# Optimization experiments

Measured on AMD Instinct MI355X. Metric: run time of the kernel, lower is better.

Reference implementation:

```python
import jax, jax.numpy as jnp
import numpy as np

VOCAB = 30001
EMB = 256
HID = 512          # bidirectional total; 256 per direction
NTAG = 9
B, L = 64, 512


def setup_inputs() -> dict:
    key = jax.random.key(0)
    ks = jax.random.split(key, 12)
    Hd = HID // 2
    s = 0.1
    return {
        "x": jax.random.randint(ks[0], (B, L), 0, VOCAB),
        "embed": jax.random.normal(ks[1], (VOCAB, EMB), jnp.float32) * s,
        "W_ih_f": jax.random.normal(ks[2], (4 * Hd, EMB), jnp.float32) * s,
        "W_hh_f": jax.random.normal(ks[3], (4 * Hd, Hd), jnp.float32) * s,
        "b_f": jax.random.normal(ks[4], (4 * Hd,), jnp.float32) * s,
        "W_ih_b": jax.random.normal(ks[5], (4 * Hd, EMB), jnp.float32) * s,
        "W_hh_b": jax.random.normal(ks[6], (4 * Hd, Hd), jnp.float32) * s,
        "b_b": jax.random.normal(ks[7], (4 * Hd,), jnp.float32) * s,
        "W_out": jax.random.normal(ks[8], (NTAG, HID), jnp.float32) * s,
        "b_out": jax.random.normal(ks[9], (NTAG,), jnp.float32) * s,
        "start_trans": jax.random.normal(ks[10], (NTAG,), jnp.float32) * s,
        "trans": jax.random.normal(ks[11], (NTAG, NTAG), jnp.float32) * s,
        "end_trans": jax.random.normal(jax.random.fold_in(key, 99), (NTAG,), jnp.float32) * s,
    }


def _lstm_dir(xg, W_hh, reverse):
    # xg: [L, B, 4H] precomputed input-to-gate projections (+ bias)
    Hd = W_hh.shape[1]
    nB = xg.shape[1]
    h0 = jnp.zeros((nB, Hd), xg.dtype)
    c0 = jnp.zeros((nB, Hd), xg.dtype)

    def step(carry, gx):
        h, c = carry
        g = gx + h @ W_hh.T                     # [B, 4H]
        i, f, gg, o = jnp.split(g, 4, axis=-1)  # torch gate order i,f,g,o
        c = jax.nn.sigmoid(f) * c + jax.nn.sigmoid(i) * jnp.tanh(gg)
        h = jax.nn.sigmoid(o) * jnp.tanh(c)
        return (h, c), h

    _, hs = jax.lax.scan(step, (h0, c0), xg, reverse=reverse)
    return hs  # [L, B, H]


def _viterbi(emissions, start, trans, end):
    # emissions: [L, B, T]. Max-plus DP (torchcrf CRF.decode, no mask).
    score0 = start + emissions[0]  # [B, T]

    def step(score, em_t):
        # score[b, i] + trans[i, j] + em_t[b, j]
        nxt = score[:, :, None] + trans[None] + em_t[:, None, :]
        return jnp.max(nxt, axis=1), jnp.argmax(nxt, axis=1)

    score, history = jax.lax.scan(step, score0, emissions[1:])  # history: [L-1, B, T]
    score = score + end
    last = jnp.argmax(score, axis=-1)   # [B] best tag at position L-1
    best = jnp.max(score, axis=-1)      # [B] best path score

    def back(tag, idx_t):
        prev = jnp.take_along_axis(idx_t, tag[:, None], axis=1)[:, 0]
        return prev, prev

    _, tags_head = jax.lax.scan(back, last, history, reverse=True)  # [L-1, B]
    tags = jnp.concatenate([tags_head, last[None]], axis=0)         # [L, B]
    return tags.T, best


def reference(x, embed, W_ih_f, W_hh_f, b_f, W_ih_b, W_hh_b, b_b,
              W_out, b_out, start_trans, trans, end_trans):
    xt = x.T                              # [L, B] time-first
    emb = embed[xt]                       # [L, B, E]
    gx_f = jnp.einsum('lbe,ge->lbg', emb, W_ih_f) + b_f
    gx_b = jnp.einsum('lbe,ge->lbg', emb, W_ih_b) + b_b
    hf = _lstm_dir(gx_f, W_hh_f, reverse=False)
    hb = _lstm_dir(gx_b, W_hh_b, reverse=True)
    outputs = jnp.concatenate([hf, hb], axis=-1)            # [L, B, HID]
    emissions = jnp.einsum('lbh,th->lbt', outputs, W_out) + b_out  # [L, B, T]
    tags, best = _viterbi(emissions, start_trans, trans, end_trans)
    return tags, best
```

## Files before the change

kernel.cpp:

```cpp
#include <hip/hip_runtime.h>
#include <math.h>


#define Bv 64
#define Lv 512

__device__ __forceinline__ float sigmoidf_(float x) { return 1.0f / (1.0f + expf(-x)); }

__global__ __launch_bounds__(256, 1) void lstm_persist(
    const int* __restrict__ x, const float* __restrict__ embed,
    const float* __restrict__ Wih_f, const float* __restrict__ Whh_f, const float* __restrict__ bf,
    const float* __restrict__ Wih_b, const float* __restrict__ Whh_b, const float* __restrict__ bb_,
    float* __restrict__ h_glob, int* __restrict__ tags, float* __restrict__ h_hist)
{
    const int bid = blockIdx.x;
    const int d  = bid >> 7;
    const int ug = (bid >> 2) & 31;
    const int bg = bid & 3;
    const int g  = d * 4 + bg;
    const int tid = threadIdx.x;
    const int u0 = ug * 8;
    const int b0 = bg * 16;

    const float* Wih  = d ? Wih_b : Wih_f;
    const float* Whh  = d ? Whh_b : Whh_f;
    const float* bias = d ? bb_   : bf;

    const int ks = tid >> 5;
    const int tr = (tid >> 2) & 7;
    const int tb = tid & 3;
    const int k0 = ks * 32;

    __shared__ float wih_lds[32][260];
    __shared__ float h_lds[16][260];
    __shared__ float emb_lds[2][16][260];
    __shared__ float parts[4][32][17];
    __shared__ float bias_lds[32];

    {
        const int row = tid >> 3;
        const int seg = tid & 7;
        const int gq = row >> 3, j = row & 7;
        const float4* src = reinterpret_cast<const float4*>(
            Wih + ((size_t)(gq * 256 + u0 + j)) * 256 + seg * 32);
        float4* dst = reinterpret_cast<float4*>(&wih_lds[row][seg * 32]);
        #pragma unroll
        for (int q = 0; q < 8; ++q) dst[q] = src[q];
    }
    if (tid < 32) bias_lds[tid] = bias[(tid >> 3) * 256 + u0 + (tid & 7)];

    float4 whh[4][8];
    #pragma unroll
    for (int i = 0; i < 4; ++i) {
        const float* wr = Whh + ((size_t)(i * 256 + u0 + tr)) * 256 + k0;
        #pragma unroll
        for (int m = 0; m < 8; ++m) whh[i][m] = *reinterpret_cast<const float4*>(wr + 4 * m);
    }

    float creg = 0.f;
    const int* my_tag = tags + g * 32 + (tid >> 3);
    int* rel_tag = tags + g * 32 + ug;

    {
        const int b = tid >> 4;
        const int cseg = tid & 15;
        const int t_eff0 = d ? (Lv - 1) : 0;
        const int xv = x[(b0 + b) * Lv + t_eff0];
        const float4* src = reinterpret_cast<const float4*>(embed + (size_t)xv * 256 + cseg * 16);
        float4* dstp = reinterpret_cast<float4*>(&emb_lds[0][b][cseg * 16]);
        dstp[0] = src[0]; dstp[1] = src[1]; dstp[2] = src[2]; dstp[3] = src[3];
    }
    __syncthreads();

    for (int tt = 0; tt < Lv; ++tt) {
        const int par = tt & 1;

        float acc[4][4];
        #pragma unroll
        for (int i = 0; i < 4; ++i)
            #pragma unroll
            for (int u = 0; u < 4; ++u) acc[i][u] = 0.f;

        #pragma unroll
        for (int m = 0; m < 8; ++m) {
            float4 ev[4];
            #pragma unroll
            for (int u = 0; u < 4; ++u)
                ev[u] = *reinterpret_cast<const float4*>(&emb_lds[par][tb + 4 * u][k0 + 4 * m]);
            #pragma unroll
            for (int i = 0; i < 4; ++i) {
                float4 wv = *reinterpret_cast<const float4*>(&wih_lds[tr + 8 * i][k0 + 4 * m]);
                #pragma unroll
                for (int u = 0; u < 4; ++u)
                    acc[i][u] += wv.x * ev[u].x + wv.y * ev[u].y + wv.z * ev[u].z + wv.w * ev[u].w;
            }
        }

        if (tt + 1 < Lv) {
            const int b = tid >> 4;
            const int cseg = tid & 15;
            const int t_eff1 = d ? (Lv - 2 - tt) : (tt + 1);
            const int xv = x[(b0 + b) * Lv + t_eff1];
            const float4* src = reinterpret_cast<const float4*>(embed + (size_t)xv * 256 + cseg * 16);
            float4 e0 = src[0], e1 = src[1], e2 = src[2], e3 = src[3];
            float4* dstp = reinterpret_cast<float4*>(&emb_lds[par ^ 1][b][cseg * 16]);
            dstp[0] = e0; dstp[1] = e1; dstp[2] = e2; dstp[3] = e3;
        }

        if (tt > 0) {
            int v, it = 0;
            for (;;) {
                asm volatile("global_load_dword %0, %1, off sc0 sc1\n\t"
                             "s_waitcnt vmcnt(0)"
                             : "=v"(v) : "v"(my_tag) : "memory");
                if (v >= tt) break;
                if (++it > (1 << 22)) break;
            }
            const float* hs = h_glob + ((size_t)par * 8 + g) * 4096 + tid * 16;
            float4 a0, a1, a2, a3;
            asm volatile(
                "global_load_dwordx4 %0, %4, off sc0 sc1\n\t"
                "global_load_dwordx4 %1, %4, off offset:16 sc0 sc1\n\t"
                "global_load_dwordx4 %2, %4, off offset:32 sc0 sc1\n\t"
                "global_load_dwordx4 %3, %4, off offset:48 sc0 sc1\n\t"
                "s_waitcnt vmcnt(0)"
                : "=v"(a0), "=v"(a1), "=v"(a2), "=v"(a3)
                : "v"(hs) : "memory");
            __builtin_amdgcn_sched_barrier(0);
            const int u = tid;
            h_lds[ 0][u] = a0.x; h_lds[ 1][u] = a0.y; h_lds[ 2][u] = a0.z; h_lds[ 3][u] = a0.w;
            h_lds[ 4][u] = a1.x; h_lds[ 5][u] = a1.y; h_lds[ 6][u] = a1.z; h_lds[ 7][u] = a1.w;
            h_lds[ 8][u] = a2.x; h_lds[ 9][u] = a2.y; h_lds[10][u] = a2.z; h_lds[11][u] = a2.w;
            h_lds[12][u] = a3.x; h_lds[13][u] = a3.y; h_lds[14][u] = a3.z; h_lds[15][u] = a3.w;
        }
        __syncthreads();

        if (tt > 0) {
            #pragma unroll
            for (int m = 0; m < 8; ++m) {
                float4 hv[4];
                #pragma unroll
                for (int u = 0; u < 4; ++u)
                    hv[u] = *reinterpret_cast<const float4*>(&h_lds[tb + 4 * u][k0 + 4 * m]);
                #pragma unroll
                for (int i = 0; i < 4; ++i) {
                    float4 wv = whh[i][m];
                    #pragma unroll
                    for (int u = 0; u < 4; ++u)
                        acc[i][u] += wv.x * hv[u].x + wv.y * hv[u].y + wv.z * hv[u].z + wv.w * hv[u].w;
                }
            }
        }

        #pragma unroll
        for (int i = 0; i < 4; ++i)
            #pragma unroll
            for (int u = 0; u < 4; ++u)
                acc[i][u] += __shfl_xor(acc[i][u], 32);
        if ((tid & 32) == 0) {
            const int w = tid >> 6;
            #pragma unroll
            for (int i = 0; i < 4; ++i)
                #pragma unroll
                for (int u = 0; u < 4; ++u)
                    parts[w][tr + 8 * i][tb + 4 * u] = acc[i][u];
        }
        __syncthreads();

        if (tid < 128) {
            const int j  = tid & 7;
            const int bb = tid >> 3;
            const int t_eff = d ? (Lv - 1 - tt) : tt;
            float gv[4];
            #pragma unroll
            for (int q = 0; q < 4; ++q) {
                const int r = q * 8 + j;
                gv[q] = parts[0][r][bb] + parts[1][r][bb] + parts[2][r][bb] + parts[3][r][bb]
                      + bias_lds[r];
            }
            creg = sigmoidf_(gv[1]) * creg + sigmoidf_(gv[0]) * tanhf(gv[2]);
            const float h = sigmoidf_(gv[3]) * tanhf(creg);
            float* dst = h_glob + ((size_t)(par ^ 1) * 8 + g) * 4096
                       + (size_t)(u0 + j) * 16 + bb;
            asm volatile("global_store_dword %0, %1, off sc0 sc1"
                         :: "v"(dst), "v"(h) : "memory");
            h_hist[((size_t)(b0 + bb) * Lv + t_eff) * 512 + d * 256 + u0 + j] = h;
        }
        asm volatile("s_waitcnt vmcnt(0)" ::: "memory");
        __syncthreads();
        if (tid == 0) {
            int val = tt + 1;
            asm volatile("global_store_dword %0, %1, off sc0 sc1"
                         :: "v"(rel_tag), "v"(val) : "memory");
        }
    }
}

__global__ __launch_bounds__(256) void emis_kernel(
    const float* __restrict__ h_hist, const float* __restrict__ Wout,
    const float* __restrict__ bout, float* __restrict__ em)
{
    const int l  = blockIdx.x >> 2;
    const int bg = blockIdx.x & 3;
    const int tid = threadIdx.x;
    __shared__ float w_lds[9][516];
    __shared__ float h_ldsx[16][512];

    for (int i = tid; i < 9 * 512; i += 256) w_lds[i >> 9][i & 511] = Wout[i];
    for (int i = tid; i < 16 * 128; i += 256) {
        const int bb = i >> 7; const int k = (i & 127) * 4;
        *reinterpret_cast<float4*>(&h_ldsx[bb][k]) =
            *reinterpret_cast<const float4*>(&h_hist[((size_t)(bg * 16 + bb) * 512 + l) * 512 + k]);
    }
    __syncthreads();

    const int bb = tid >> 4;
    const int j = tid & 15;
    if (j < 9) {
        float acc = bout[j];
        #pragma unroll 4
        for (int k = 0; k < 512; k += 4) {
            float4 hv = *reinterpret_cast<const float4*>(&h_ldsx[bb][k]);
            float4 wv = *reinterpret_cast<const float4*>(&w_lds[j][k]);
            acc += hv.x * wv.x + hv.y * wv.y + hv.z * wv.z + hv.w * wv.w;
        }
        em[((size_t)l * 64 + bg * 16 + bb) * 9 + j] = acc;
    }
}

__global__ __launch_bounds__(576) void viterbi_fwd(
    const float* __restrict__ em, const float* __restrict__ start,
    const float* __restrict__ trans, const float* __restrict__ endt,
    unsigned char* __restrict__ hist, int* __restrict__ last_tag,
    float* __restrict__ out_best)
{
    const int tid = threadIdx.x;
    const int b = tid / 9;
    const int j = tid - b * 9;
    __shared__ float sc[2][64][9];
    float t9[9];
    #pragma unroll
    for (int i = 0; i < 9; ++i) t9[i] = trans[i * 9 + j];

    sc[0][b][j] = start[j] + em[tid];
    float emv = em[(64 + b) * 9 + j];
    __syncthreads();
    for (int t = 1; t < 512; ++t) {
        float em_nxt = (t < 511) ? em[((t + 1) * 64 + b) * 9 + j] : 0.f;
        const int cur = t & 1, prv = cur ^ 1;
        float best = -1e30f; int arg = 0;
        #pragma unroll
        for (int i = 0; i < 9; ++i) {
            float v = sc[prv][b][i] + t9[i];
            if (v > best) { best = v; arg = i; }
        }
        best += emv;
        sc[cur][b][j] = best;
        hist[((size_t)b * 512 + t) * 9 + j] = (unsigned char)arg;
        __syncthreads();
        emv = em_nxt;
    }
    sc[1][b][j] += endt[j];
    __syncthreads();
    if (j == 0) {
        float best = -1e30f; int arg = 0;
        #pragma unroll
        for (int i = 0; i < 9; ++i) {
            float v = sc[1][b][i];
            if (v > best) { best = v; arg = i; }
        }
        out_best[b] = best;
        last_tag[b] = arg;
    }
}

__global__ __launch_bounds__(256) void backtrack(
    const unsigned char* __restrict__ hist, const int* __restrict__ last_tag,
    float* __restrict__ out_tags)
{
    const int b = blockIdx.x;
    const int tid = threadIdx.x;
    __shared__ __align__(16) unsigned char hl[512 * 9];
    const uint4* src = reinterpret_cast<const uint4*>(hist + (size_t)b * 512 * 9);
    uint4* dst = reinterpret_cast<uint4*>(hl);
    for (int i = tid; i < 512 * 9 / 16; i += 256) dst[i] = src[i];
    __syncthreads();
    if (tid == 0) {
        int tag = last_tag[b];
        out_tags[b * 512 + 511] = (float)tag;
        for (int t = 511; t >= 1; --t) {
            tag = hl[t * 9 + tag];
            out_tags[b * 512 + t - 1] = (float)tag;
        }
    }
}

extern "C" void kernel_launch(void* const* d_in, const int* in_sizes, int n_in,
                              void* d_out, int out_size, void* d_ws, size_t ws_size,
                              hipStream_t stream)
{
    const int*   x     = (const int*)d_in[0];
    const float* embed = (const float*)d_in[1];
    const float* Wih_f = (const float*)d_in[2];
    const float* Whh_f = (const float*)d_in[3];
    const float* bf    = (const float*)d_in[4];
    const float* Wih_b = (const float*)d_in[5];
    const float* Whh_b = (const float*)d_in[6];
    const float* bb    = (const float*)d_in[7];
    const float* Wout  = (const float*)d_in[8];
    const float* bout  = (const float*)d_in[9];
    const float* start = (const float*)d_in[10];
    const float* trans = (const float*)d_in[11];
    const float* endt  = (const float*)d_in[12];

    char* ws = (char*)d_ws;
    float* h_glob = (float*)ws;
    int*   tags   = (int*)(ws + 262144);
    float* h_hist = (float*)(ws + 266240);
    float* em     = (float*)(ws + 266240 + 67108864);
    int*   last_tag = (int*)(ws + 67375104 + 1179648);
    unsigned char* hist = (unsigned char*)(ws + 68554752 + 256);

    float* out = (float*)d_out;

    hipMemsetAsync(tags, 0, 4096, stream);

    lstm_persist<<<256, 256, 0, stream>>>(x, embed, Wih_f, Whh_f, bf,
                                          Wih_b, Whh_b, bb,
                                          h_glob, tags, h_hist);
    emis_kernel<<<2048, 256, 0, stream>>>(h_hist, Wout, bout, em);
    viterbi_fwd<<<1, 576, 0, stream>>>(em, start, trans, endt, hist, last_tag, out + 64 * 512);
    backtrack<<<64, 256, 0, stream>>>(hist, last_tag, out);
}
```

Before: 2.852 ms.

## Rework persistent LSTM cross-block sync with per-wave flags and double-buffered h

Reassigns block IDs so blocks of the same group are interleaved, and double-buffers the shared h tile so the block-wide barrier before releasing the step flag can be dropped. Each wave now publishes its own progress flag (four per block), and consumers poll all four with a single vector load, sleeping briefly after a few failed polls. The h_hist store is moved after the flag release so it leaves the critical path, and the cell update is spread over even threads in all waves. The aim is lower per-timestep synchronization latency in the 512-step recurrence, at the cost of more complex flag ordering and slightly more LDS.

```diff
diff --git a/kernel.cpp b/kernel.cpp
--- a/kernel.cpp
+++ b/kernel.cpp
@@ -14,10 +14,10 @@
     float* __restrict__ h_glob, int* __restrict__ tags, float* __restrict__ h_hist)
 {
     const int bid = blockIdx.x;
-    const int d  = bid >> 7;
-    const int ug = (bid >> 2) & 31;
-    const int bg = bid & 3;
-    const int g  = d * 4 + bg;
+    const int g  = bid & 7;
+    const int d  = g >> 2;
+    const int bg = g & 3;
+    const int ug = bid >> 3;
     const int tid = threadIdx.x;
     const int u0 = ug * 8;
     const int b0 = bg * 16;
@@ -32,7 +32,7 @@
     const int k0 = ks * 32;
 
     __shared__ float wih_lds[32][260];
-    __shared__ float h_lds[16][260];
+    __shared__ float h_lds[2][16][260];
     __shared__ float emb_lds[2][16][260];
     __shared__ float parts[4][32][17];
     __shared__ float bias_lds[32];
@@ -56,10 +56,6 @@
         #pragma unroll
         for (int m = 0; m < 8; ++m) whh[i][m] = *reinterpret_cast<const float4*>(wr + 4 * m);
     }
-
-    float creg = 0.f;
-    const int* my_tag = tags + g * 32 + (tid >> 3);
-    int* rel_tag = tags + g * 32 + ug;
 
     {
         const int b = tid >> 4;
@@ -71,6 +67,10 @@
         dstp[0] = src[0]; dstp[1] = src[1]; dstp[2] = src[2]; dstp[3] = src[3];
     }
     __syncthreads();
+
+    float creg = 0.f;
+    const int* my_tags = tags + ((g * 32 + (tid >> 3)) << 2);
+    int* rel_tag = tags + ((g * 32 + ug) << 2) + (tid >> 6);
 
     for (int tt = 0; tt < Lv; ++tt) {
         const int par = tt & 1;
@@ -108,15 +108,15 @@
         }
 
         if (tt > 0) {
-            int v, it = 0;
+            int4 tv; int it = 0;
             for (;;) {
-                asm volatile("global_load_dword %0, %1, off sc0 sc1\n\t"
-                             "s_waitcnt vmcnt(0)"
-                             : "=v"(v) : "v"(my_tag) : "memory");
-                if (v >= tt) break;
-                if (++it > (1 << 22)) break;
+                asm volatile("global_load_dwordx4 %0, %1, off sc0 sc1\n\ts_waitcnt vmcnt(0)"
+                             : "=v"(tv) : "v"(my_tags) : "memory");
+                if (tv.x >= tt && tv.y >= tt && tv.z >= tt && tv.w >= tt) break;
+                if (++it > 2) __builtin_amdgcn_s_sleep(2);
+                if (it > (1 << 22)) break;
             }
-            const float* hs = h_glob + ((size_t)par * 8 + g) * 4096 + tid * 16;
+            const float* hs = h_glob + ((size_t)(g * 2 + par)) * 4096 + tid * 16;
             float4 a0, a1, a2, a3;
             asm volatile(
                 "global_load_dwordx4 %0, %4, off sc0 sc1\n\t"
@@ -124,14 +124,12 @@
                 "global_load_dwordx4 %2, %4, off offset:32 sc0 sc1\n\t"
                 "global_load_dwordx4 %3, %4, off offset:48 sc0 sc1\n\t"
                 "s_waitcnt vmcnt(0)"
-                : "=v"(a0), "=v"(a1), "=v"(a2), "=v"(a3)
-                : "v"(hs) : "memory");
-            __builtin_amdgcn_sched_barrier(0);
+                : "=v"(a0), "=v"(a1), "=v"(a2), "=v"(a3) : "v"(hs) : "memory");
             const int u = tid;
-            h_lds[ 0][u] = a0.x; h_lds[ 1][u] = a0.y; h_lds[ 2][u] = a0.z; h_lds[ 3][u] = a0.w;
-            h_lds[ 4][u] = a1.x; h_lds[ 5][u] = a1.y; h_lds[ 6][u] = a1.z; h_lds[ 7][u] = a1.w;
-            h_lds[ 8][u] = a2.x; h_lds[ 9][u] = a2.y; h_lds[10][u] = a2.z; h_lds[11][u] = a2.w;
-            h_lds[12][u] = a3.x; h_lds[13][u] = a3.y; h_lds[14][u] = a3.z; h_lds[15][u] = a3.w;
+            h_lds[par][ 0][u] = a0.x; h_lds[par][ 1][u] = a0.y; h_lds[par][ 2][u] = a0.z; h_lds[par][ 3][u] = a0.w;
+            h_lds[par][ 4][u] = a1.x; h_lds[par][ 5][u] = a1.y; h_lds[par][ 6][u] = a1.z; h_lds[par][ 7][u] = a1.w;
+            h_lds[par][ 8][u] = a2.x; h_lds[par][ 9][u] = a2.y; h_lds[par][10][u] = a2.z; h_lds[par][11][u] = a2.w;
+            h_lds[par][12][u] = a3.x; h_lds[par][13][u] = a3.y; h_lds[par][14][u] = a3.z; h_lds[par][15][u] = a3.w;
         }
         __syncthreads();
 
@@ -141,7 +139,7 @@
                 float4 hv[4];
                 #pragma unroll
                 for (int u = 0; u < 4; ++u)
-                    hv[u] = *reinterpret_cast<const float4*>(&h_lds[tb + 4 * u][k0 + 4 * m]);
+                    hv[u] = *reinterpret_cast<const float4*>(&h_lds[par][tb + 4 * u][k0 + 4 * m]);
                 #pragma unroll
                 for (int i = 0; i < 4; ++i) {
                     float4 wv = whh[i][m];
@@ -167,10 +165,11 @@
         }
         __syncthreads();
 
-        if (tid < 128) {
-            const int j  = tid & 7;
-            const int bb = tid >> 3;
-            const int t_eff = d ? (Lv - 1 - tt) : tt;
+        float hval = 0.f;
+        if (!(tid & 1)) {
+            const int p  = tid >> 1;
+            const int j  = p & 7;
+            const int bb = p >> 3;
             float gv[4];
             #pragma unroll
             for (int q = 0; q < 4; ++q) {
@@ -179,19 +178,23 @@
                       + bias_lds[r];
             }
             creg = sigmoidf_(gv[1]) * creg + sigmoidf_(gv[0]) * tanhf(gv[2]);
-            const float h = sigmoidf_(gv[3]) * tanhf(creg);
-            float* dst = h_glob + ((size_t)(par ^ 1) * 8 + g) * 4096
-                       + (size_t)(u0 + j) * 16 + bb;
+            hval = sigmoidf_(gv[3]) * tanhf(creg);
+            float* dst = h_glob + ((size_t)(g * 2 + (par ^ 1))) * 4096 + (u0 + j) * 16 + bb;
             asm volatile("global_store_dword %0, %1, off sc0 sc1"
-                         :: "v"(dst), "v"(h) : "memory");
-            h_hist[((size_t)(b0 + bb) * Lv + t_eff) * 512 + d * 256 + u0 + j] = h;
+                         :: "v"(dst), "v"(hval) : "memory");
         }
         asm volatile("s_waitcnt vmcnt(0)" ::: "memory");
-        __syncthreads();
-        if (tid == 0) {
+        if ((tid & 63) == 0) {
             int val = tt + 1;
             asm volatile("global_store_dword %0, %1, off sc0 sc1"
                          :: "v"(rel_tag), "v"(val) : "memory");
+        }
+        if (!(tid & 1)) {
+            const int p  = tid >> 1;
+            const int j  = p & 7;
+            const int bb = p >> 3;
+            const int t_eff = d ? (Lv - 1 - tt) : tt;
+            h_hist[((size_t)(b0 + bb) * Lv + t_eff) * 512 + d * 256 + u0 + j] = hval;
         }
     }
 }
@@ -314,12 +317,12 @@
     const float* endt  = (const float*)d_in[12];
 
     char* ws = (char*)d_ws;
-    float* h_glob = (float*)ws;
-    int*   tags   = (int*)(ws + 262144);
-    float* h_hist = (float*)(ws + 266240);
-    float* em     = (float*)(ws + 266240 + 67108864);
-    int*   last_tag = (int*)(ws + 67375104 + 1179648);
-    unsigned char* hist = (unsigned char*)(ws + 68554752 + 256);
+    float* h_glob  = (float*)ws;
+    int*   tags    = (int*)(ws + 262144);
+    float* h_hist  = (float*)(ws + 267264);
+    float* em      = (float*)(ws + 267264 + 67108864);
+    int*   last_tag = (int*)(ws + 68555776);
+    unsigned char* hist = (unsigned char*)(ws + 68556032);
 
     float* out = (float*)d_out;
 
```

New measurement: 2.817 ms. No clear change (-1.2%).
